# Kernel tuning notes

Hardware: AMD Instinct MI355X
Metric: run time of the kernel (lower is better)

Reference implementation:

```python
import jax, jax.numpy as jnp
import numpy as np

TAU = 2.0      # LIF membrane time constant
ALPHA = 4.0    # spikingjelly surrogate.Sigmoid default alpha
EPS = 1e-5     # BatchNorm eps
HEADS = 8

@jax.custom_vjp
def heaviside(x):
    return (x >= 0).astype(x.dtype)

def _hv_fwd(x):
    return (x >= 0).astype(x.dtype), x

def _hv_bwd(x, g):
    s = jax.nn.sigmoid(ALPHA * x)
    return (g * ALPHA * s * (1.0 - s),)

heaviside.defvjp(_hv_fwd, _hv_bwd)

def lif(x, vth=1.0):
    # multi-step LIF, decay_input=True, v_reset=0 (hard reset), detach_reset=True
    def step(v, xt):
        v = v + (xt - v) / TAU
        s = heaviside(v - vth)
        v = v * (1.0 - jax.lax.stop_gradient(s))
        return v, s
    _, spikes = jax.lax.scan(step, jnp.zeros_like(x[0]), x)
    return spikes

def bn(x, gamma, beta, mean, var):
    # x: [T,B,C,N]; eval-mode BatchNorm1d over channel axis 2
    inv = gamma * jax.lax.rsqrt(var + EPS)
    return x * inv[None, None, :, None] + (beta - mean * inv)[None, None, :, None]

def conv1x1(x, w):
    # x: [T,B,C,N], w: [Cout,Cin] (Conv1d kernel_size=1)
    return jnp.einsum('tbcn,dc->tbdn', x, w)

def setup_inputs():
    key = jax.random.key(0)
    ks = jax.random.split(key, 24)
    T, B, C, H, W = 4, 16, 512, 32, 32
    scale = 1.0 / np.sqrt(C)
    d = {}
    d['x'] = jax.random.normal(ks[0], (T, B, C, H, W), jnp.float32)
    def bn_params(i):
        g = 1.0 + 0.1 * jax.random.normal(ks[i], (C,), jnp.float32)
        b = 0.1 * jax.random.normal(ks[i + 1], (C,), jnp.float32)
        m = 0.1 * jax.random.normal(ks[i + 2], (C,), jnp.float32)
        v = jax.random.uniform(ks[i + 3], (C,), jnp.float32, 0.5, 1.5)
        return g, b, m, v
    d['q_w'] = scale * jax.random.normal(ks[1], (C, C), jnp.float32)
    d['q_gamma'], d['q_beta'], d['q_mean'], d['q_var'] = bn_params(2)
    d['k_w'] = scale * jax.random.normal(ks[6], (C, C), jnp.float32)
    d['k_gamma'], d['k_beta'], d['k_mean'], d['k_var'] = bn_params(7)
    d['proj_w'] = scale * jax.random.normal(ks[11], (C, C), jnp.float32)
    d['proj_b'] = 0.01 * jax.random.normal(ks[12], (C,), jnp.float32)
    d['p_gamma'], d['p_beta'], d['p_mean'], d['p_var'] = bn_params(13)
    return d

def reference(x, q_w, q_gamma, q_beta, q_mean, q_var,
              k_w, k_gamma, k_beta, k_mean, k_var,
              proj_w, proj_b, p_gamma, p_beta, p_mean, p_var):
    T, B, C, H, W = x.shape
    N = H * W
    Dh = C // HEADS
    xs = lif(x).reshape(T, B, C, N)                    # shortcut_lif then flatten(3)
    q = lif(bn(conv1x1(xs, q_w), q_gamma, q_beta, q_mean, q_var))
    k = lif(bn(conv1x1(xs, k_w), k_gamma, k_beta, k_mean, k_var))
    qh = q.reshape(T, B, HEADS, Dh, N).sum(axis=3, keepdims=True)  # [T,B,h,1,N]
    attn = lif(qh, vth=0.5)
    kh = k.reshape(T, B, HEADS, Dh, N)
    y = (attn * kh).reshape(T, B, C, N)
    y = bn(conv1x1(y, proj_w) + proj_b[None, None, :, None],
           p_gamma, p_beta, p_mean, p_var)
    return y.reshape(T, B, C, H, W), attn
```

## Files before the change

### kernel.cpp

```cpp
#include <hip/hip_runtime.h>

typedef unsigned short u16;
typedef unsigned int u32;
typedef float f32x4 __attribute__((ext_vector_type(4)));
typedef short s16x8 __attribute__((ext_vector_type(8)));

#define T_ 4
#define B_ 16
#define C_ 512
#define N_ 1024
#define YSZ 33554432

__device__ __forceinline__ u16 f2bf(float f) {
  u32 u = __float_as_uint(f);
  u32 r = u + 0x7FFFu + ((u >> 16) & 1u);
  return (u16)(r >> 16);
}
__device__ __forceinline__ float bf2f(u16 h) { return __uint_as_float(((u32)h) << 16); }

__device__ __forceinline__ void async16(const void* g, void* l) {
  __builtin_amdgcn_global_load_lds((const __attribute__((address_space(1))) void*)g,
                                   (__attribute__((address_space(3))) void*)l, 16, 0, 0);
}

__global__ void prep_kernel(const float* __restrict__ qw, const float* __restrict__ kw,
                            const float* __restrict__ pw,
                            const float* __restrict__ qg, const float* __restrict__ qb,
                            const float* __restrict__ qm, const float* __restrict__ qv,
                            const float* __restrict__ kg, const float* __restrict__ kb,
                            const float* __restrict__ km, const float* __restrict__ kv,
                            const float* __restrict__ pg, const float* __restrict__ pbt,
                            const float* __restrict__ pm, const float* __restrict__ pv,
                            u16* __restrict__ whlq, u16* __restrict__ whlk,
                            u16* __restrict__ pwb, float* __restrict__ consts) {
  int blk = blockIdx.x, tid = threadIdx.x;
  if (blk < 512) {
    int d = blk;
    for (int c = tid; c < 512; c += 256) {
      float w = qw[d * 512 + c];
      u16 hi = f2bf(w);
      whlq[d * 1024 + c] = hi;
      whlq[d * 1024 + 512 + c] = f2bf(w - bf2f(hi));
      w = kw[d * 512 + c];
      hi = f2bf(w);
      whlk[d * 1024 + c] = hi;
      whlk[d * 1024 + 512 + c] = f2bf(w - bf2f(hi));
      pwb[d * 512 + c] = f2bf(pw[d * 512 + c]);
    }
  } else {
    for (int c = tid; c < 512; c += 256) {
      float inv = qg[c] / sqrtf(qv[c] + 1e-5f);
      consts[c] = inv; consts[512 + c] = qb[c] - qm[c] * inv;
      inv = kg[c] / sqrtf(kv[c] + 1e-5f);
      consts[1024 + c] = inv; consts[1536 + c] = kb[c] - km[c] * inv;
      inv = pg[c] / sqrtf(pv[c] + 1e-5f);
      consts[2048 + c] = inv; consts[2560 + c] = pbt[c] - pm[c] * inv;
    }
  }
}

__global__ __launch_bounds__(256) void lifx_kernel(const float* __restrict__ x,
                                                   u16* __restrict__ xs) {
  int b = blockIdx.z;
  int cbase = blockIdx.y * 64, nbase = blockIdx.x * 64;
  int tid = threadIdx.x;
  int c_l = tid >> 6, n_l = tid & 63;
  __shared__ __align__(16) u16 tile[64 * 72];
  float v[16];
#pragma unroll
  for (int i = 0; i < 16; ++i) v[i] = 0.f;
  for (int t = 0; t < 4; ++t) {
    const float* xp = x + ((size_t)(t * 16 + b) * 512 + cbase + c_l * 16) * 1024 + nbase + n_l;
#pragma unroll
    for (int i = 0; i < 16; ++i) {
      float xv = xp[(size_t)i * 1024];
      float vn = v[i] + 0.5f * (xv - v[i]);
      bool s = vn >= 1.0f;
      tile[n_l * 72 + c_l * 16 + i] = s ? 0x3F80 : 0;
      v[i] = s ? 0.f : vn;
    }
    __syncthreads();
    u16* yb = xs + ((size_t)(t * 16 + b) * 1024 + nbase) * 512 + cbase;
#pragma unroll
    for (int e = 0; e < 2; ++e) {
      int chunk = tid * 2 + e;
      int n = chunk >> 3, c0 = (chunk & 7) * 8;
      *(uint4*)&yb[(size_t)n * 512 + c0] = *(const uint4*)&tile[n * 72 + c0];
    }
    __syncthreads();
  }
}

__global__ __launch_bounds__(256, 2) void gemm_q_kernel(
    const u16* __restrict__ A, const u16* __restrict__ Bbase,
    const float* __restrict__ consts, float* __restrict__ dout) {
  const int tid = threadIdx.x;
  const int lane = tid & 63, w = tid >> 6;
  const int wm = w >> 1, wn = w & 1;
  const int quad = lane >> 4, l16 = lane & 15;
  const int b = blockIdx.z;
  const int m_blk = blockIdx.y * 128, n_blk = blockIdx.x * 128;
  const int srow = lane >> 3;
  const int scol = (((lane & 7) ^ srow) & 7) * 8;
  __shared__ __align__(16) u16 smem[3 * 128 * 64];
  u16* Ash = smem;
  u16* Asl = smem + 8192;
  u16* Bs  = smem + 16384;
  const int rxor = l16 & 7;
  float v[64];
#pragma unroll
  for (int i = 0; i < 64; ++i) v[i] = 0.f;
  float va[4] = {0.f, 0.f, 0.f, 0.f};

  for (int t = 0; t < 4; ++t) {
    f32x4 acc[4][4];
    const f32x4 zero = {0.f, 0.f, 0.f, 0.f};
#pragma unroll
    for (int i = 0; i < 4; ++i)
#pragma unroll
      for (int j = 0; j < 4; ++j) acc[i][j] = zero;
    const u16* Bt = Bbase + (size_t)(t * 16 + b) * (N_ * C_);

    for (int k0 = 0; k0 < 512; k0 += 64) {
#pragma unroll
      for (int i = 0; i < 4; ++i) {
        int r = i * 32 + w * 8 + srow;
        int lo = (i * 32 + w * 8) * 64;
        async16(A + (size_t)(m_blk + r) * 1024 + k0 + scol, &Ash[lo]);
        async16(A + (size_t)(m_blk + r) * 1024 + 512 + k0 + scol, &Asl[lo]);
        async16(Bt + (size_t)(n_blk + r) * 512 + k0 + scol, &Bs[lo]);
      }
      __syncthreads();
#pragma unroll
      for (int kk = 0; kk < 2; ++kk) {
        s16x8 ah[4], al[4], bf[4];
        const int slot = ((kk * 4 + quad) ^ rxor) * 8;
#pragma unroll
        for (int ti = 0; ti < 4; ++ti) {
          ah[ti] = *(const s16x8*)&Ash[(wm * 64 + ti * 16 + l16) * 64 + slot];
          al[ti] = *(const s16x8*)&Asl[(wm * 64 + ti * 16 + l16) * 64 + slot];
        }
#pragma unroll
        for (int tj = 0; tj < 4; ++tj)
          bf[tj] = *(const s16x8*)&Bs[(wn * 64 + tj * 16 + l16) * 64 + slot];
#pragma unroll
        for (int ti = 0; ti < 4; ++ti)
#pragma unroll
          for (int tj = 0; tj < 4; ++tj) {
            acc[ti][tj] = __builtin_amdgcn_mfma_f32_16x16x32_bf16(ah[ti], bf[tj], acc[ti][tj], 0, 0, 0);
            acc[ti][tj] = __builtin_amdgcn_mfma_f32_16x16x32_bf16(al[ti], bf[tj], acc[ti][tj], 0, 0, 0);
          }
      }
      __syncthreads();
    }

    float qp[4] = {0.f, 0.f, 0.f, 0.f};
#pragma unroll
    for (int ti = 0; ti < 4; ++ti) {
#pragma unroll
      for (int r = 0; r < 4; ++r) {
        int row = m_blk + wm * 64 + ti * 16 + quad * 4 + r;
        float iv = consts[row], ib = consts[512 + row];
#pragma unroll
        for (int tj = 0; tj < 4; ++tj) {
          float bnv = acc[ti][tj][r] * iv + ib;
          float vv = v[(ti * 4 + tj) * 4 + r];
          float vn = vv + 0.5f * (bnv - vv);
          bool s = vn >= 1.0f;
          v[(ti * 4 + tj) * 4 + r] = s ? 0.f : vn;
          qp[tj] += s ? 1.f : 0.f;
        }
      }
    }
    int h = (m_blk >> 6) + wm;
#pragma unroll
    for (int tj = 0; tj < 4; ++tj) {
      float q = qp[tj];
      q += __shfl_xor(q, 16, 64);
      q += __shfl_xor(q, 32, 64);
      float vn = va[tj] + 0.5f * (q - va[tj]);
      bool s = vn >= 0.5f;
      va[tj] = s ? 0.f : vn;
      if (quad == 0) {
        int col = n_blk + wn * 64 + tj * 16 + l16;
        dout[(size_t)YSZ + ((size_t)(t * 16 + b) * 8 + h) * 1024 + col] = s ? 1.f : 0.f;
      }
    }
  }
}

__global__ __launch_bounds__(256, 2) void gemm_k_kernel(
    const u16* __restrict__ A, const u16* __restrict__ Bbase,
    const float* __restrict__ consts, const float* __restrict__ dout,
    u16* __restrict__ y) {
  const int tid = threadIdx.x;
  const int lane = tid & 63, w = tid >> 6;
  const int wm = w >> 1, wn = w & 1;
  const int quad = lane >> 4, l16 = lane & 15;
  const int b = blockIdx.z;
  const int m_blk = blockIdx.y * 128, n_blk = blockIdx.x * 128;
  const int srow = lane >> 3;
  const int scol = (((lane & 7) ^ srow) & 7) * 8;
  __shared__ __align__(16) u16 smem[3 * 128 * 64];
  u16* Ash = smem;
  u16* Asl = smem + 8192;
  u16* Bs  = smem + 16384;
  u16* Ys  = smem;
  const int rxor = l16 & 7;
  float v[64];
#pragma unroll
  for (int i = 0; i < 64; ++i) v[i] = 0.f;

  for (int t = 0; t < 4; ++t) {
    f32x4 acc[4][4];
    const f32x4 zero = {0.f, 0.f, 0.f, 0.f};
#pragma unroll
    for (int i = 0; i < 4; ++i)
#pragma unroll
      for (int j = 0; j < 4; ++j) acc[i][j] = zero;
    const u16* Bt = Bbase + (size_t)(t * 16 + b) * (N_ * C_);

    for (int k0 = 0; k0 < 512; k0 += 64) {
#pragma unroll
      for (int i = 0; i < 4; ++i) {
        int r = i * 32 + w * 8 + srow;
        int lo = (i * 32 + w * 8) * 64;
        async16(A + (size_t)(m_blk + r) * 1024 + k0 + scol, &Ash[lo]);
        async16(A + (size_t)(m_blk + r) * 1024 + 512 + k0 + scol, &Asl[lo]);
        async16(Bt + (size_t)(n_blk + r) * 512 + k0 + scol, &Bs[lo]);
      }
      __syncthreads();
#pragma unroll
      for (int kk = 0; kk < 2; ++kk) {
        s16x8 ah[4], al[4], bf[4];
        const int slot = ((kk * 4 + quad) ^ rxor) * 8;
#pragma unroll
        for (int ti = 0; ti < 4; ++ti) {
          ah[ti] = *(const s16x8*)&Ash[(wm * 64 + ti * 16 + l16) * 64 + slot];
          al[ti] = *(const s16x8*)&Asl[(wm * 64 + ti * 16 + l16) * 64 + slot];
        }
#pragma unroll
        for (int tj = 0; tj < 4; ++tj)
          bf[tj] = *(const s16x8*)&Bs[(wn * 64 + tj * 16 + l16) * 64 + slot];
#pragma unroll
        for (int ti = 0; ti < 4; ++ti)
#pragma unroll
          for (int tj = 0; tj < 4; ++tj) {
            acc[ti][tj] = __builtin_amdgcn_mfma_f32_16x16x32_bf16(ah[ti], bf[tj], acc[ti][tj], 0, 0, 0);
            acc[ti][tj] = __builtin_amdgcn_mfma_f32_16x16x32_bf16(al[ti], bf[tj], acc[ti][tj], 0, 0, 0);
          }
      }
      __syncthreads();
    }

    int h = (m_blk >> 6) + wm;
    float at[4];
#pragma unroll
    for (int tj = 0; tj < 4; ++tj) {
      int col = n_blk + wn * 64 + tj * 16 + l16;
      at[tj] = dout[(size_t)YSZ + ((size_t)(t * 16 + b) * 8 + h) * 1024 + col];
    }

#pragma unroll
    for (int ti = 0; ti < 4; ++ti) {
      u16 pk[4][4];
#pragma unroll
      for (int r = 0; r < 4; ++r) {
        int row = m_blk + wm * 64 + ti * 16 + quad * 4 + r;
        float iv = consts[1024 + row], ib = consts[1536 + row];
#pragma unroll
        for (int tj = 0; tj < 4; ++tj) {
          float bnv = acc[ti][tj][r] * iv + ib;
          float vv = v[(ti * 4 + tj) * 4 + r];
          float vn = vv + 0.5f * (bnv - vv);
          bool s = vn >= 1.0f;
          v[(ti * 4 + tj) * 4 + r] = s ? 0.f : vn;
          pk[tj][r] = (s && at[tj] != 0.f) ? 0x3F80 : 0;
        }
      }
#pragma unroll
      for (int tj = 0; tj < 4; ++tj) {
        int n_loc = wn * 64 + tj * 16 + l16;
        int c_loc = wm * 64 + ti * 16 + quad * 4;
        u32 lo2 = (u32)pk[tj][0] | ((u32)pk[tj][1] << 16);
        u32 hi2 = (u32)pk[tj][2] | ((u32)pk[tj][3] << 16);
        uint2 pv2; pv2.x = lo2; pv2.y = hi2;
        *(uint2*)&Ys[n_loc * 132 + c_loc] = pv2;
      }
    }
    __syncthreads();
    u16* yb = y + ((size_t)(t * 16 + b) * 1024 + n_blk) * 512 + m_blk;
#pragma unroll
    for (int p = 0; p < 8; ++p) {
      int idx = p * 256 + tid;
      int rown = idx >> 4, ch = (idx & 15) * 8;
      *(uint4*)&yb[(size_t)rown * 512 + ch] = *(const uint4*)&Ys[rown * 132 + ch];
    }
    __syncthreads();
  }
}

__global__ __launch_bounds__(256, 3) void gemm_proj_kernel(
    const u16* __restrict__ A, const u16* __restrict__ Bbase,
    float* __restrict__ outP, const float* __restrict__ projb,
    const float* __restrict__ consts) {
  const int tid = threadIdx.x;
  const int lane = tid & 63, w = tid >> 6;
  const int wm = w >> 1, wn = w & 1;
  const int quad = lane >> 4, l16 = lane & 15;
  const int tb = blockIdx.z;
  const int m_blk = blockIdx.y * 128, n_blk = blockIdx.x * 128;
  const int srow = lane >> 3;
  const int scol = (((lane & 7) ^ srow) & 7) * 8;
  __shared__ __align__(16) u16 As[128 * 64];
  __shared__ __align__(16) u16 Bs[128 * 64];
  f32x4 acc[4][4];
  const f32x4 zero = {0.f, 0.f, 0.f, 0.f};
#pragma unroll
  for (int i = 0; i < 4; ++i)
#pragma unroll
    for (int j = 0; j < 4; ++j) acc[i][j] = zero;
  const u16* Bt = Bbase + (size_t)tb * (N_ * C_);
  const int rxor = l16 & 7;

  for (int k0 = 0; k0 < 512; k0 += 64) {
#pragma unroll
    for (int i = 0; i < 4; ++i) {
      int r = i * 32 + w * 8 + srow;
      async16(A + (size_t)(m_blk + r) * 512 + k0 + scol, &As[(i * 32 + w * 8) * 64]);
      async16(Bt + (size_t)(n_blk + r) * 512 + k0 + scol, &Bs[(i * 32 + w * 8) * 64]);
    }
    __syncthreads();
#pragma unroll
    for (int kk = 0; kk < 2; ++kk) {
      s16x8 af[4], bf[4];
      const int slot = ((kk * 4 + quad) ^ rxor) * 8;
#pragma unroll
      for (int ti = 0; ti < 4; ++ti)
        af[ti] = *(const s16x8*)&As[(wm * 64 + ti * 16 + l16) * 64 + slot];
#pragma unroll
      for (int tj = 0; tj < 4; ++tj)
        bf[tj] = *(const s16x8*)&Bs[(wn * 64 + tj * 16 + l16) * 64 + slot];
#pragma unroll
      for (int ti = 0; ti < 4; ++ti)
#pragma unroll
        for (int tj = 0; tj < 4; ++tj)
          acc[ti][tj] = __builtin_amdgcn_mfma_f32_16x16x32_bf16(af[ti], bf[tj], acc[ti][tj], 0, 0, 0);
    }
    __syncthreads();
  }

  const float* pinv = consts + 2048;
  const float* pb2 = consts + 2560;
  float* o = outP + (size_t)tb * (C_ * N_);
#pragma unroll
  for (int ti = 0; ti < 4; ++ti) {
    int row0 = m_blk + wm * 64 + ti * 16 + quad * 4;
#pragma unroll
    for (int r = 0; r < 4; ++r) {
      int row = row0 + r;
      float bi = projb[row], piv = pinv[row], pbi = pb2[row];
#pragma unroll
      for (int tj = 0; tj < 4; ++tj) {
        int col = n_blk + wn * 64 + tj * 16 + l16;
        o[(size_t)row * N_ + col] = (acc[ti][tj][r] + bi) * piv + pbi;
      }
    }
  }
}

extern "C" void kernel_launch(void* const* d_in, const int* in_sizes, int n_in,
                              void* d_out, int out_size, void* d_ws, size_t ws_size,
                              hipStream_t stream) {
  const float* x   = (const float*)d_in[0];
  const float* qw  = (const float*)d_in[1];
  const float* qg  = (const float*)d_in[2];
  const float* qb  = (const float*)d_in[3];
  const float* qm  = (const float*)d_in[4];
  const float* qv  = (const float*)d_in[5];
  const float* kw  = (const float*)d_in[6];
  const float* kg  = (const float*)d_in[7];
  const float* kb  = (const float*)d_in[8];
  const float* km  = (const float*)d_in[9];
  const float* kv  = (const float*)d_in[10];
  const float* pw  = (const float*)d_in[11];
  const float* pb  = (const float*)d_in[12];
  const float* pg  = (const float*)d_in[13];
  const float* pbt = (const float*)d_in[14];
  const float* pm  = (const float*)d_in[15];
  const float* pv  = (const float*)d_in[16];
  float* out = (float*)d_out;
  char* ws = (char*)d_ws;

  u16* xs       = (u16*)ws;
  u16* y2       = (u16*)(ws + 67108864);
  u16* whlq     = (u16*)(ws + 201326592);
  u16* whlk     = (u16*)(ws + 202375168);
  u16* pwb      = (u16*)(ws + 203423744);
  float* consts = (float*)(ws + 203948032);

  prep_kernel<<<513, 256, 0, stream>>>(qw, kw, pw, qg, qb, qm, qv, kg, kb, km, kv,
                                       pg, pbt, pm, pv, whlq, whlk, pwb, consts);
  lifx_kernel<<<dim3(16, 8, 16), 256, 0, stream>>>(x, xs);
  gemm_q_kernel<<<dim3(8, 4, 16), 256, 0, stream>>>(whlq, xs, consts, out);
  gemm_k_kernel<<<dim3(8, 4, 16), 256, 0, stream>>>(whlk, xs, consts, out, y2);
  gemm_proj_kernel<<<dim3(8, 4, 64), 256, 0, stream>>>(pwb, y2, out, pb, consts);
}
```

Before: 430.5 us.

## Fuse Q and K GEMMs into one kernel sharing the xs tile

Merges the separate Q and K conv GEMM kernels into one 512-thread kernel. Warps 0-3 compute Q and warps 4-7 compute K on the same staged B (xs) tile, so xs is loaded from global memory once instead of twice. The attention spikes pass to the K warps through shared memory rather than a global round trip, and one kernel launch is removed. In exchange the kernel uses more shared memory (80KB) and larger blocks, which can lower occupancy, and adds an extra barrier per timestep.

```diff
diff --git a/kernel.cpp b/kernel.cpp
--- a/kernel.cpp
+++ b/kernel.cpp
@@ -91,21 +91,31 @@
   }
 }
 
-__global__ __launch_bounds__(256, 2) void gemm_q_kernel(
-    const u16* __restrict__ A, const u16* __restrict__ Bbase,
-    const float* __restrict__ consts, float* __restrict__ dout) {
+__global__ __launch_bounds__(512, 2) void gemm_qk_kernel(
+    const u16* __restrict__ Aq, const u16* __restrict__ Ak,
+    const u16* __restrict__ Bbase, const float* __restrict__ consts,
+    float* __restrict__ dout, u16* __restrict__ y) {
   const int tid = threadIdx.x;
   const int lane = tid & 63, w = tid >> 6;
-  const int wm = w >> 1, wn = w & 1;
+  const bool isQ = w < 4;
+  const int rw = isQ ? w : (w - 4);
+  const int wm = rw >> 1, wn = rw & 1;
   const int quad = lane >> 4, l16 = lane & 15;
   const int b = blockIdx.z;
   const int m_blk = blockIdx.y * 128, n_blk = blockIdx.x * 128;
   const int srow = lane >> 3;
   const int scol = (((lane & 7) ^ srow) & 7) * 8;
-  __shared__ __align__(16) u16 smem[3 * 128 * 64];
-  u16* Ash = smem;
-  u16* Asl = smem + 8192;
-  u16* Bs  = smem + 16384;
+  __shared__ __align__(16) u16 smem[40960];
+  u16* Aqh = smem;
+  u16* Aql = smem + 8192;
+  u16* Akh = smem + 16384;
+  u16* Akl = smem + 24576;
+  u16* Bs  = smem + 32768;
+  float* attn_s = (float*)(smem + 32768);
+  u16* Ys = smem;
+  u16* Ah = isQ ? Aqh : Akh;
+  u16* Al = isQ ? Aql : Akl;
+  const int cb = isQ ? 0 : 1024;
   const int rxor = l16 & 7;
   float v[64];
 #pragma unroll
@@ -123,11 +133,14 @@
 
     for (int k0 = 0; k0 < 512; k0 += 64) {
 #pragma unroll
-      for (int i = 0; i < 4; ++i) {
-        int r = i * 32 + w * 8 + srow;
-        int lo = (i * 32 + w * 8) * 64;
-        async16(A + (size_t)(m_blk + r) * 1024 + k0 + scol, &Ash[lo]);
-        async16(A + (size_t)(m_blk + r) * 1024 + 512 + k0 + scol, &Asl[lo]);
+      for (int j = 0; j < 2; ++j) {
+        int r = j * 64 + w * 8 + srow;
+        int lo = (j * 64 + w * 8) * 64;
+        const size_t ar = (size_t)(m_blk + r) * 1024 + k0 + scol;
+        async16(Aq + ar,       &Aqh[lo]);
+        async16(Aq + ar + 512, &Aql[lo]);
+        async16(Ak + ar,       &Akh[lo]);
+        async16(Ak + ar + 512, &Akl[lo]);
         async16(Bt + (size_t)(n_blk + r) * 512 + k0 + scol, &Bs[lo]);
       }
       __syncthreads();
@@ -137,8 +150,8 @@
         const int slot = ((kk * 4 + quad) ^ rxor) * 8;
 #pragma unroll
         for (int ti = 0; ti < 4; ++ti) {
-          ah[ti] = *(const s16x8*)&Ash[(wm * 64 + ti * 16 + l16) * 64 + slot];
-          al[ti] = *(const s16x8*)&Asl[(wm * 64 + ti * 16 + l16) * 64 + slot];
+          ah[ti] = *(const s16x8*)&Ah[(wm * 64 + ti * 16 + l16) * 64 + slot];
+          al[ti] = *(const s16x8*)&Al[(wm * 64 + ti * 16 + l16) * 64 + slot];
         }
 #pragma unroll
         for (int tj = 0; tj < 4; ++tj)
@@ -154,145 +167,82 @@
       __syncthreads();
     }
 
-    float qp[4] = {0.f, 0.f, 0.f, 0.f};
-#pragma unroll
-    for (int ti = 0; ti < 4; ++ti) {
-#pragma unroll
-      for (int r = 0; r < 4; ++r) {
-        int row = m_blk + wm * 64 + ti * 16 + quad * 4 + r;
-        float iv = consts[row], ib = consts[512 + row];
+    if (isQ) {
+      float qp[4] = {0.f, 0.f, 0.f, 0.f};
+#pragma unroll
+      for (int ti = 0; ti < 4; ++ti) {
+#pragma unroll
+        for (int r = 0; r < 4; ++r) {
+          int row = m_blk + wm * 64 + ti * 16 + quad * 4 + r;
+          float iv = consts[row], ib = consts[512 + row];
+#pragma unroll
+          for (int tj = 0; tj < 4; ++tj) {
+            float bnv = acc[ti][tj][r] * iv + ib;
+            float vv = v[(ti * 4 + tj) * 4 + r];
+            float vn = vv + 0.5f * (bnv - vv);
+            bool s = vn >= 1.0f;
+            v[(ti * 4 + tj) * 4 + r] = s ? 0.f : vn;
+            qp[tj] += s ? 1.f : 0.f;
+          }
+        }
+      }
+      int h = (m_blk >> 6) + wm;
+#pragma unroll
+      for (int tj = 0; tj < 4; ++tj) {
+        float q = qp[tj];
+        q += __shfl_xor(q, 16, 64);
+        q += __shfl_xor(q, 32, 64);
+        float vn = va[tj] + 0.5f * (q - va[tj]);
+        bool s = vn >= 0.5f;
+        va[tj] = s ? 0.f : vn;
+        if (quad == 0) {
+          int cl = wn * 64 + tj * 16 + l16;
+          float sv = s ? 1.f : 0.f;
+          attn_s[wm * 128 + cl] = sv;
+          dout[(size_t)YSZ + ((size_t)(t * 16 + b) * 8 + h) * 1024 + n_blk + cl] = sv;
+        }
+      }
+    }
+    __syncthreads();
+
+    if (!isQ) {
+      float at[4];
+#pragma unroll
+      for (int tj = 0; tj < 4; ++tj)
+        at[tj] = attn_s[wm * 128 + wn * 64 + tj * 16 + l16];
+#pragma unroll
+      for (int ti = 0; ti < 4; ++ti) {
+        u16 pk[4][4];
+#pragma unroll
+        for (int r = 0; r < 4; ++r) {
+          int row = m_blk + wm * 64 + ti * 16 + quad * 4 + r;
+          float iv = consts[cb + row], ib = consts[cb + 512 + row];
+#pragma unroll
+          for (int tj = 0; tj < 4; ++tj) {
+            float bnv = acc[ti][tj][r] * iv + ib;
+            float vv = v[(ti * 4 + tj) * 4 + r];
+            float vn = vv + 0.5f * (bnv - vv);
+            bool s = vn >= 1.0f;
+            v[(ti * 4 + tj) * 4 + r] = s ? 0.f : vn;
+            pk[tj][r] = (s && at[tj] != 0.f) ? 0x3F80 : 0;
+          }
+        }
 #pragma unroll
         for (int tj = 0; tj < 4; ++tj) {
-          float bnv = acc[ti][tj][r] * iv + ib;
-          float vv = v[(ti * 4 + tj) * 4 + r];
-          float vn = vv + 0.5f * (bnv - vv);
-          bool s = vn >= 1.0f;
-          v[(ti * 4 + tj) * 4 + r] = s ? 0.f : vn;
-          qp[tj] += s ? 1.f : 0.f;
-        }
-      }
-    }
-    int h = (m_blk >> 6) + wm;
-#pragma unroll
-    for (int tj = 0; tj < 4; ++tj) {
-      float q = qp[tj];
-      q += __shfl_xor(q, 16, 64);
-      q += __shfl_xor(q, 32, 64);
-      float vn = va[tj] + 0.5f * (q - va[tj]);
-      bool s = vn >= 0.5f;
-      va[tj] = s ? 0.f : vn;
-      if (quad == 0) {
-        int col = n_blk + wn * 64 + tj * 16 + l16;
-        dout[(size_t)YSZ + ((size_t)(t * 16 + b) * 8 + h) * 1024 + col] = s ? 1.f : 0.f;
-      }
-    }
-  }
-}
-
-__global__ __launch_bounds__(256, 2) void gemm_k_kernel(
-    const u16* __restrict__ A, const u16* __restrict__ Bbase,
-    const float* __restrict__ consts, const float* __restrict__ dout,
-    u16* __restrict__ y) {
-  const int tid = threadIdx.x;
-  const int lane = tid & 63, w = tid >> 6;
-  const int wm = w >> 1, wn = w & 1;
-  const int quad = lane >> 4, l16 = lane & 15;
-  const int b = blockIdx.z;
-  const int m_blk = blockIdx.y * 128, n_blk = blockIdx.x * 128;
-  const int srow = lane >> 3;
-  const int scol = (((lane & 7) ^ srow) & 7) * 8;
-  __shared__ __align__(16) u16 smem[3 * 128 * 64];
-  u16* Ash = smem;
-  u16* Asl = smem + 8192;
-  u16* Bs  = smem + 16384;
-  u16* Ys  = smem;
-  const int rxor = l16 & 7;
-  float v[64];
-#pragma unroll
-  for (int i = 0; i < 64; ++i) v[i] = 0.f;
-
-  for (int t = 0; t < 4; ++t) {
-    f32x4 acc[4][4];
-    const f32x4 zero = {0.f, 0.f, 0.f, 0.f};
-#pragma unroll
-    for (int i = 0; i < 4; ++i)
-#pragma unroll
-      for (int j = 0; j < 4; ++j) acc[i][j] = zero;
-    const u16* Bt = Bbase + (size_t)(t * 16 + b) * (N_ * C_);
-
-    for (int k0 = 0; k0 < 512; k0 += 64) {
-#pragma unroll
-      for (int i = 0; i < 4; ++i) {
-        int r = i * 32 + w * 8 + srow;
-        int lo = (i * 32 + w * 8) * 64;
-        async16(A + (size_t)(m_blk + r) * 1024 + k0 + scol, &Ash[lo]);
-        async16(A + (size_t)(m_blk + r) * 1024 + 512 + k0 + scol, &Asl[lo]);
-        async16(Bt + (size_t)(n_blk + r) * 512 + k0 + scol, &Bs[lo]);
-      }
-      __syncthreads();
-#pragma unroll
-      for (int kk = 0; kk < 2; ++kk) {
-        s16x8 ah[4], al[4], bf[4];
-        const int slot = ((kk * 4 + quad) ^ rxor) * 8;
-#pragma unroll
-        for (int ti = 0; ti < 4; ++ti) {
-          ah[ti] = *(const s16x8*)&Ash[(wm * 64 + ti * 16 + l16) * 64 + slot];
-          al[ti] = *(const s16x8*)&Asl[(wm * 64 + ti * 16 + l16) * 64 + slot];
-        }
-#pragma unroll
-        for (int tj = 0; tj < 4; ++tj)
-          bf[tj] = *(const s16x8*)&Bs[(wn * 64 + tj * 16 + l16) * 64 + slot];
-#pragma unroll
-        for (int ti = 0; ti < 4; ++ti)
-#pragma unroll
-          for (int tj = 0; tj < 4; ++tj) {
-            acc[ti][tj] = __builtin_amdgcn_mfma_f32_16x16x32_bf16(ah[ti], bf[tj], acc[ti][tj], 0, 0, 0);
-            acc[ti][tj] = __builtin_amdgcn_mfma_f32_16x16x32_bf16(al[ti], bf[tj], acc[ti][tj], 0, 0, 0);
-          }
-      }
-      __syncthreads();
-    }
-
-    int h = (m_blk >> 6) + wm;
-    float at[4];
-#pragma unroll
-    for (int tj = 0; tj < 4; ++tj) {
-      int col = n_blk + wn * 64 + tj * 16 + l16;
-      at[tj] = dout[(size_t)YSZ + ((size_t)(t * 16 + b) * 8 + h) * 1024 + col];
-    }
-
-#pragma unroll
-    for (int ti = 0; ti < 4; ++ti) {
-      u16 pk[4][4];
-#pragma unroll
-      for (int r = 0; r < 4; ++r) {
-        int row = m_blk + wm * 64 + ti * 16 + quad * 4 + r;
-        float iv = consts[1024 + row], ib = consts[1536 + row];
-#pragma unroll
-        for (int tj = 0; tj < 4; ++tj) {
-          float bnv = acc[ti][tj][r] * iv + ib;
-          float vv = v[(ti * 4 + tj) * 4 + r];
-          float vn = vv + 0.5f * (bnv - vv);
-          bool s = vn >= 1.0f;
-          v[(ti * 4 + tj) * 4 + r] = s ? 0.f : vn;
-          pk[tj][r] = (s && at[tj] != 0.f) ? 0x3F80 : 0;
-        }
-      }
-#pragma unroll
-      for (int tj = 0; tj < 4; ++tj) {
-        int n_loc = wn * 64 + tj * 16 + l16;
-        int c_loc = wm * 64 + ti * 16 + quad * 4;
-        u32 lo2 = (u32)pk[tj][0] | ((u32)pk[tj][1] << 16);
-        u32 hi2 = (u32)pk[tj][2] | ((u32)pk[tj][3] << 16);
-        uint2 pv2; pv2.x = lo2; pv2.y = hi2;
-        *(uint2*)&Ys[n_loc * 132 + c_loc] = pv2;
+          int n_loc = wn * 64 + tj * 16 + l16;
+          int c_loc = wm * 64 + ti * 16 + quad * 4;
+          u32 lo2 = (u32)pk[tj][0] | ((u32)pk[tj][1] << 16);
+          u32 hi2 = (u32)pk[tj][2] | ((u32)pk[tj][3] << 16);
+          uint2 pv2; pv2.x = lo2; pv2.y = hi2;
+          *(uint2*)&Ys[n_loc * 132 + c_loc] = pv2;
+        }
       }
     }
     __syncthreads();
     u16* yb = y + ((size_t)(t * 16 + b) * 1024 + n_blk) * 512 + m_blk;
 #pragma unroll
-    for (int p = 0; p < 8; ++p) {
-      int idx = p * 256 + tid;
+    for (int p = 0; p < 4; ++p) {
+      int idx = p * 512 + tid;
       int rown = idx >> 4, ch = (idx & 15) * 8;
       *(uint4*)&yb[(size_t)rown * 512 + ch] = *(const uint4*)&Ys[rown * 132 + ch];
     }
@@ -402,7 +352,6 @@
   prep_kernel<<<513, 256, 0, stream>>>(qw, kw, pw, qg, qb, qm, qv, kg, kb, km, kv,
                                        pg, pbt, pm, pv, whlq, whlk, pwb, consts);
   lifx_kernel<<<dim3(16, 8, 16), 256, 0, stream>>>(x, xs);
-  gemm_q_kernel<<<dim3(8, 4, 16), 256, 0, stream>>>(whlq, xs, consts, out);
-  gemm_k_kernel<<<dim3(8, 4, 16), 256, 0, stream>>>(whlk, xs, consts, out, y2);
+  gemm_qk_kernel<<<dim3(8, 4, 16), 512, 0, stream>>>(whlq, whlk, xs, consts, out, y2);
   gemm_proj_kernel<<<dim3(8, 4, 64), 256, 0, stream>>>(pwb, y2, out, pb, consts);
 }
```

After: 467.7 us. 1.09x slower.

## Pre-pack weights into MFMA fragment order and load A operands directly from global

Applied to the files above, without the earlier changes.

The prep kernel now writes the q/k hi/lo split weights and the projection weights in a per-lane MFMA fragment layout. The GEMM kernels then read A fragments straight from global memory (L2-cached) as 16-byte vector loads instead of staging them through LDS. This cuts LDS footprint and the async copy traffic for A, which may allow better occupancy. In exchange, A loads are now synchronous global loads inside the inner loop, which could add latency stalls.

```diff
diff --git a/kernel.cpp b/kernel.cpp
--- a/kernel.cpp
+++ b/kernel.cpp
@@ -31,21 +31,24 @@
                             const float* __restrict__ km, const float* __restrict__ kv,
                             const float* __restrict__ pg, const float* __restrict__ pbt,
                             const float* __restrict__ pm, const float* __restrict__ pv,
-                            u16* __restrict__ whlq, u16* __restrict__ whlk,
-                            u16* __restrict__ pwb, float* __restrict__ consts) {
+                            u16* __restrict__ pq, u16* __restrict__ pk_,
+                            u16* __restrict__ pp, float* __restrict__ consts) {
   int blk = blockIdx.x, tid = threadIdx.x;
   if (blk < 512) {
     int d = blk;
+    int rt = d >> 4, l16r = d & 15;
     for (int c = tid; c < 512; c += 256) {
+      int ck = c >> 5, quad = (c >> 3) & 3, j = c & 7;
+      size_t lane8 = (size_t)(quad * 16 + l16r) * 8 + j;
       float w = qw[d * 512 + c];
       u16 hi = f2bf(w);
-      whlq[d * 1024 + c] = hi;
-      whlq[d * 1024 + 512 + c] = f2bf(w - bf2f(hi));
+      pq[((size_t)(rt * 32 + ck)) * 512 + lane8] = hi;
+      pq[((size_t)(rt * 32 + ck + 16)) * 512 + lane8] = f2bf(w - bf2f(hi));
       w = kw[d * 512 + c];
       hi = f2bf(w);
-      whlk[d * 1024 + c] = hi;
-      whlk[d * 1024 + 512 + c] = f2bf(w - bf2f(hi));
-      pwb[d * 512 + c] = f2bf(pw[d * 512 + c]);
+      pk_[((size_t)(rt * 32 + ck)) * 512 + lane8] = hi;
+      pk_[((size_t)(rt * 32 + ck + 16)) * 512 + lane8] = f2bf(w - bf2f(hi));
+      pp[((size_t)(rt * 16 + ck)) * 512 + lane8] = f2bf(pw[d * 512 + c]);
     }
   } else {
     for (int c = tid; c < 512; c += 256) {
@@ -92,7 +95,7 @@
 }
 
 __global__ __launch_bounds__(256, 2) void gemm_q_kernel(
-    const u16* __restrict__ A, const u16* __restrict__ Bbase,
+    const u16* __restrict__ Afrag, const u16* __restrict__ Bbase,
     const float* __restrict__ consts, float* __restrict__ dout) {
   const int tid = threadIdx.x;
   const int lane = tid & 63, w = tid >> 6;
@@ -102,11 +105,9 @@
   const int m_blk = blockIdx.y * 128, n_blk = blockIdx.x * 128;
   const int srow = lane >> 3;
   const int scol = (((lane & 7) ^ srow) & 7) * 8;
-  __shared__ __align__(16) u16 smem[3 * 128 * 64];
-  u16* Ash = smem;
-  u16* Asl = smem + 8192;
-  u16* Bs  = smem + 16384;
+  __shared__ __align__(16) u16 Bs[128 * 64];
   const int rxor = l16 & 7;
+  const u16* Abase = Afrag + ((size_t)(blockIdx.y * 8 + wm * 4) * 32) * 512 + (size_t)lane * 8;
   float v[64];
 #pragma unroll
   for (int i = 0; i < 64; ++i) v[i] = 0.f;
@@ -125,20 +126,18 @@
 #pragma unroll
       for (int i = 0; i < 4; ++i) {
         int r = i * 32 + w * 8 + srow;
-        int lo = (i * 32 + w * 8) * 64;
-        async16(A + (size_t)(m_blk + r) * 1024 + k0 + scol, &Ash[lo]);
-        async16(A + (size_t)(m_blk + r) * 1024 + 512 + k0 + scol, &Asl[lo]);
-        async16(Bt + (size_t)(n_blk + r) * 512 + k0 + scol, &Bs[lo]);
+        async16(Bt + (size_t)(n_blk + r) * 512 + k0 + scol, &Bs[(i * 32 + w * 8) * 64]);
       }
       __syncthreads();
+      const int ckb = k0 >> 5;
 #pragma unroll
       for (int kk = 0; kk < 2; ++kk) {
         s16x8 ah[4], al[4], bf[4];
         const int slot = ((kk * 4 + quad) ^ rxor) * 8;
 #pragma unroll
         for (int ti = 0; ti < 4; ++ti) {
-          ah[ti] = *(const s16x8*)&Ash[(wm * 64 + ti * 16 + l16) * 64 + slot];
-          al[ti] = *(const s16x8*)&Asl[(wm * 64 + ti * 16 + l16) * 64 + slot];
+          ah[ti] = *(const s16x8*)(Abase + ((size_t)(ti * 32 + ckb + kk)) * 512);
+          al[ti] = *(const s16x8*)(Abase + ((size_t)(ti * 32 + ckb + kk + 16)) * 512);
         }
 #pragma unroll
         for (int tj = 0; tj < 4; ++tj)
@@ -190,7 +189,7 @@
 }
 
 __global__ __launch_bounds__(256, 2) void gemm_k_kernel(
-    const u16* __restrict__ A, const u16* __restrict__ Bbase,
+    const u16* __restrict__ Afrag, const u16* __restrict__ Bbase,
     const float* __restrict__ consts, const float* __restrict__ dout,
     u16* __restrict__ y) {
   const int tid = threadIdx.x;
@@ -201,12 +200,11 @@
   const int m_blk = blockIdx.y * 128, n_blk = blockIdx.x * 128;
   const int srow = lane >> 3;
   const int scol = (((lane & 7) ^ srow) & 7) * 8;
-  __shared__ __align__(16) u16 smem[3 * 128 * 64];
-  u16* Ash = smem;
-  u16* Asl = smem + 8192;
-  u16* Bs  = smem + 16384;
-  u16* Ys  = smem;
+  __shared__ __align__(16) u16 smem[128 * 132];
+  u16* Bs = smem;
+  u16* Ys = smem;
   const int rxor = l16 & 7;
+  const u16* Abase = Afrag + ((size_t)(blockIdx.y * 8 + wm * 4) * 32) * 512 + (size_t)lane * 8;
   float v[64];
 #pragma unroll
   for (int i = 0; i < 64; ++i) v[i] = 0.f;
@@ -224,20 +222,18 @@
 #pragma unroll
       for (int i = 0; i < 4; ++i) {
         int r = i * 32 + w * 8 + srow;
-        int lo = (i * 32 + w * 8) * 64;
-        async16(A + (size_t)(m_blk + r) * 1024 + k0 + scol, &Ash[lo]);
-        async16(A + (size_t)(m_blk + r) * 1024 + 512 + k0 + scol, &Asl[lo]);
-        async16(Bt + (size_t)(n_blk + r) * 512 + k0 + scol, &Bs[lo]);
+        async16(Bt + (size_t)(n_blk + r) * 512 + k0 + scol, &Bs[(i * 32 + w * 8) * 64]);
       }
       __syncthreads();
+      const int ckb = k0 >> 5;
 #pragma unroll
       for (int kk = 0; kk < 2; ++kk) {
         s16x8 ah[4], al[4], bf[4];
         const int slot = ((kk * 4 + quad) ^ rxor) * 8;
 #pragma unroll
         for (int ti = 0; ti < 4; ++ti) {
-          ah[ti] = *(const s16x8*)&Ash[(wm * 64 + ti * 16 + l16) * 64 + slot];
-          al[ti] = *(const s16x8*)&Asl[(wm * 64 + ti * 16 + l16) * 64 + slot];
+          ah[ti] = *(const s16x8*)(Abase + ((size_t)(ti * 32 + ckb + kk)) * 512);
+          al[ti] = *(const s16x8*)(Abase + ((size_t)(ti * 32 + ckb + kk + 16)) * 512);
         }
 #pragma unroll
         for (int tj = 0; tj < 4; ++tj)
@@ -301,7 +297,7 @@
 }
 
 __global__ __launch_bounds__(256, 3) void gemm_proj_kernel(
-    const u16* __restrict__ A, const u16* __restrict__ Bbase,
+    const u16* __restrict__ Afrag, const u16* __restrict__ Bbase,
     float* __restrict__ outP, const float* __restrict__ projb,
     const float* __restrict__ consts) {
   const int tid = threadIdx.x;
@@ -312,7 +308,6 @@
   const int m_blk = blockIdx.y * 128, n_blk = blockIdx.x * 128;
   const int srow = lane >> 3;
   const int scol = (((lane & 7) ^ srow) & 7) * 8;
-  __shared__ __align__(16) u16 As[128 * 64];
   __shared__ __align__(16) u16 Bs[128 * 64];
   f32x4 acc[4][4];
   const f32x4 zero = {0.f, 0.f, 0.f, 0.f};
@@ -321,23 +316,24 @@
 #pragma unroll
     for (int j = 0; j < 4; ++j) acc[i][j] = zero;
   const u16* Bt = Bbase + (size_t)tb * (N_ * C_);
+  const u16* Abase = Afrag + ((size_t)(blockIdx.y * 8 + wm * 4) * 16) * 512 + (size_t)lane * 8;
   const int rxor = l16 & 7;
 
   for (int k0 = 0; k0 < 512; k0 += 64) {
 #pragma unroll
     for (int i = 0; i < 4; ++i) {
       int r = i * 32 + w * 8 + srow;
-      async16(A + (size_t)(m_blk + r) * 512 + k0 + scol, &As[(i * 32 + w * 8) * 64]);
       async16(Bt + (size_t)(n_blk + r) * 512 + k0 + scol, &Bs[(i * 32 + w * 8) * 64]);
     }
     __syncthreads();
+    const int ckb = k0 >> 5;
 #pragma unroll
     for (int kk = 0; kk < 2; ++kk) {
       s16x8 af[4], bf[4];
       const int slot = ((kk * 4 + quad) ^ rxor) * 8;
 #pragma unroll
       for (int ti = 0; ti < 4; ++ti)
-        af[ti] = *(const s16x8*)&As[(wm * 64 + ti * 16 + l16) * 64 + slot];
+        af[ti] = *(const s16x8*)(Abase + ((size_t)(ti * 16 + ckb + kk)) * 512);
 #pragma unroll
       for (int tj = 0; tj < 4; ++tj)
         bf[tj] = *(const s16x8*)&Bs[(wn * 64 + tj * 16 + l16) * 64 + slot];
@@ -394,15 +390,15 @@
 
   u16* xs       = (u16*)ws;
   u16* y2       = (u16*)(ws + 67108864);
-  u16* whlq     = (u16*)(ws + 201326592);
-  u16* whlk     = (u16*)(ws + 202375168);
-  u16* pwb      = (u16*)(ws + 203423744);
+  u16* pq       = (u16*)(ws + 201326592);
+  u16* pk_      = (u16*)(ws + 202375168);
+  u16* pp       = (u16*)(ws + 203423744);
   float* consts = (float*)(ws + 203948032);
 
   prep_kernel<<<513, 256, 0, stream>>>(qw, kw, pw, qg, qb, qm, qv, kg, kb, km, kv,
-                                       pg, pbt, pm, pv, whlq, whlk, pwb, consts);
+                                       pg, pbt, pm, pv, pq, pk_, pp, consts);
   lifx_kernel<<<dim3(16, 8, 16), 256, 0, stream>>>(x, xs);
-  gemm_q_kernel<<<dim3(8, 4, 16), 256, 0, stream>>>(whlq, xs, consts, out);
-  gemm_k_kernel<<<dim3(8, 4, 16), 256, 0, stream>>>(whlk, xs, consts, out, y2);
-  gemm_proj_kernel<<<dim3(8, 4, 64), 256, 0, stream>>>(pwb, y2, out, pb, consts);
-}
+  gemm_q_kernel<<<dim3(8, 4, 16), 256, 0, stream>>>(pq, xs, consts, out);
+  gemm_k_kernel<<<dim3(8, 4, 16), 256, 0, stream>>>(pk_, xs, consts, out, y2);
+  gemm_proj_kernel<<<dim3(8, 4, 64), 256, 0, stream>>>(pp, y2, out, pb, consts);
+}
```

Result: slower. 565.6 us (+31.4%).
